# Optimization experiments

Measured on AMD Instinct MI355X. Metric: run time of the kernel, lower is better.

The kernel has to match this reference:

```python
import jax, jax.numpy as jnp
import numpy as np

N_NODES = 100000
N_EDGES = 1200000
F_IN, F_HID, F_OUT = 64, 16, 40


def setup_inputs() -> dict:
    key = jax.random.key(0)
    ks = jax.random.split(key, 6)
    x = jax.random.normal(ks[0], (N_NODES, F_IN), dtype=jnp.float32)
    edge_index = jax.random.randint(ks[1], (2, N_EDGES), 0, N_NODES, dtype=jnp.int32)
    s1 = 1.0 / np.sqrt(F_IN)
    s2 = 1.0 / np.sqrt(F_HID)
    return {
        "x": x,
        "edge_index": edge_index,
        "W1_self": jax.random.normal(ks[2], (F_IN, F_HID), dtype=jnp.float32) * s1,
        "W1_neigh": jax.random.normal(ks[3], (F_IN, F_HID), dtype=jnp.float32) * s1,
        "b1": jnp.zeros((F_HID,), dtype=jnp.float32),
        "W2_self": jax.random.normal(ks[4], (F_HID, F_OUT), dtype=jnp.float32) * s2,
        "W2_neigh": jax.random.normal(ks[5], (F_HID, F_OUT), dtype=jnp.float32) * s2,
        "b2": jnp.zeros((F_OUT,), dtype=jnp.float32),
    }


def _sage_conv(x, src, dst, W_self, W_neigh, b):
    # gather source features along edges, mean-aggregate onto destinations
    n = x.shape[0]
    deg = jax.ops.segment_sum(jnp.ones((src.shape[0],), x.dtype), dst, num_segments=n)
    agg = jax.ops.segment_sum(x[src], dst, num_segments=n)
    agg = agg / jnp.maximum(deg, 1.0)[:, None]
    return x @ W_self + agg @ W_neigh + b


def reference(x, edge_index, W1_self, W1_neigh, b1, W2_self, W2_neigh, b2):
    src, dst = edge_index[0], edge_index[1]
    h = jax.nn.relu(_sage_conv(x, src, dst, W1_self, W1_neigh, b1))
    # F.dropout with training=False is identity (eval-mode reference)
    out = _sage_conv(h, src, dst, W2_self, W2_neigh, b2)
    return jax.nn.log_softmax(out, axis=1)
```

## Files before the change

### kernel.cpp

```cpp
#include <hip/hip_runtime.h>
#include <math.h>

#define N_NODES 100000
#define N_EDGES 1200000
#define F_IN    64
#define F_HID   16
#define F_OUT   40

#define BK_SHIFT 7
#define BK_NODES 128
#define NB 782
#define CAP 1792
#define S1_EPB 8192
#define BIN_BLOCKS ((N_EDGES + S1_EPB - 1) / S1_EPB)
#define GEMM_BLOCKS ((N_NODES + 15) / 16)

typedef _Float16 v2h __attribute__((ext_vector_type(2)));

__global__ __launch_bounds__(256)
void k1_bin_gemm(const int* __restrict__ src, const int* __restrict__ dst,
                 unsigned* __restrict__ cursor, unsigned* __restrict__ csr,
                 const float* __restrict__ x, const float* __restrict__ Wn,
                 const float* __restrict__ Ws, const float* __restrict__ b1,
                 _Float16* __restrict__ t1, _Float16* __restrict__ xs, int nE) {
    __shared__ __align__(16) char smem[12416];
    int tid = threadIdx.x;
    int bid = blockIdx.x;
    if (bid < BIN_BLOCKS) {
        unsigned* cnt = (unsigned*)smem;
        for (int i = tid; i < NB; i += 256) cnt[i] = 0u;
        __syncthreads();
        int tb = bid * S1_EPB + tid * 32;
        if (tb + 32 <= nE) {
            const int4* d4 = (const int4*)(dst + tb);
#pragma unroll
            for (int j = 0; j < 8; j++) {
                int4 v = d4[j];
                atomicAdd(&cnt[((unsigned)v.x) >> BK_SHIFT], 1u);
                atomicAdd(&cnt[((unsigned)v.y) >> BK_SHIFT], 1u);
                atomicAdd(&cnt[((unsigned)v.z) >> BK_SHIFT], 1u);
                atomicAdd(&cnt[((unsigned)v.w) >> BK_SHIFT], 1u);
            }
        } else {
            for (int e = tb; e < nE && e < tb + 32; e++)
                atomicAdd(&cnt[((unsigned)dst[e]) >> BK_SHIFT], 1u);
        }
        __syncthreads();
        for (int i = tid; i < NB; i += 256) {
            unsigned c = cnt[i];
            cnt[i] = c ? atomicAdd(&cursor[i], c) : 0u;
        }
        __syncthreads();
        if (tb + 32 <= nE) {
            const int4* d4 = (const int4*)(dst + tb);
            const int4* s4 = (const int4*)(src + tb);
#pragma unroll
            for (int j = 0; j < 8; j++) {
                int4 dv = d4[j];
                int4 sv = s4[j];
                int da[4] = {dv.x, dv.y, dv.z, dv.w};
                int sa[4] = {sv.x, sv.y, sv.z, sv.w};
#pragma unroll
                for (int q = 0; q < 4; q++) {
                    unsigned d = (unsigned)da[q];
                    unsigned b = d >> BK_SHIFT;
                    unsigned pos = atomicAdd(&cnt[b], 1u);
                    if (pos < CAP)
                        csr[b * CAP + pos] = (((unsigned)sa[q]) << BK_SHIFT) | (d & (BK_NODES - 1));
                }
            }
        } else {
            for (int e = tb; e < nE && e < tb + 32; e++) {
                unsigned d = (unsigned)dst[e];
                unsigned b = d >> BK_SHIFT;
                unsigned pos = atomicAdd(&cnt[b], 1u);
                if (pos < CAP)
                    csr[b * CAP + pos] = (((unsigned)src[e]) << BK_SHIFT) | (d & (BK_NODES - 1));
            }
        }
    } else {
        float* sWn = (float*)smem;
        float* sWs = sWn + 1024;
        float* sb  = sWs + 1024;
        float* sx  = sb + 16;
        for (int i = tid; i < F_IN * F_HID; i += 256) { sWn[i] = Wn[i]; sWs[i] = Ws[i]; }
        if (tid < F_HID) sb[tid] = b1[tid];
        int row0 = (bid - BIN_BLOCKS) * 16;
        const float* xg = x + (size_t)row0 * F_IN;
        for (int i = tid; i < 16 * F_IN; i += 256)
            sx[(i >> 6) * 65 + (i & 63)] = xg[i];
        __syncthreads();
        int r = tid >> 4, c = tid & 15;
        int row = row0 + r;
        const float* xr = sx + r * 65;
        float sn = 0.f, ss = sb[c];
#pragma unroll
        for (int k = 0; k < F_IN; k++) {
            float xv = xr[k];
            sn += xv * sWn[k * F_HID + c];
            ss += xv * sWs[k * F_HID + c];
        }
        t1[row * F_HID + c] = (_Float16)sn;
        xs[row * F_HID + c] = (_Float16)ss;
    }
}

__global__ __launch_bounds__(256)
void k2_csr_sort(const unsigned* __restrict__ cursor, unsigned* __restrict__ csr,
                 unsigned* __restrict__ node_info) {
    __shared__ unsigned words[CAP];
    __shared__ unsigned hist[BK_NODES];
    __shared__ unsigned lcur[BK_NODES];
    int tid = threadIdx.x;
    int b = blockIdx.x;
    unsigned count = cursor[b]; if (count > CAP) count = CAP;
    unsigned* reg = csr + (size_t)b * CAP;
    for (unsigned i = tid; i < count; i += 256) words[i] = reg[i];
    for (int i = tid; i < BK_NODES; i += 256) hist[i] = 0u;
    __syncthreads();
    for (unsigned i = tid; i < count; i += 256)
        atomicAdd(&hist[words[i] & (BK_NODES - 1)], 1u);
    __syncthreads();
    unsigned hv = (tid < BK_NODES) ? hist[tid] : 0u;
    __syncthreads();
    for (int d = 1; d < BK_NODES; d <<= 1) {
        unsigned t = (tid < BK_NODES && tid >= d) ? hist[tid - d] : 0u;
        __syncthreads();
        if (tid < BK_NODES) hist[tid] += t;
        __syncthreads();
    }
    if (tid < BK_NODES) {
        unsigned excl = hist[tid] - hv;
        int node = (b << BK_SHIFT) + tid;
        if (node < N_NODES) node_info[node] = (excl << 16) | hv;
        lcur[tid] = excl;
    }
    __syncthreads();
    for (unsigned i = tid; i < count; i += 256) {
        unsigned w = words[i];
        unsigned pos = atomicAdd(&lcur[w & (BK_NODES - 1)], 1u);
        reg[pos] = w >> BK_SHIFT;
    }
}

__global__ __launch_bounds__(256)
void agg1_kernel(const unsigned* __restrict__ node_info, const unsigned* __restrict__ csr,
                 const _Float16* __restrict__ t1, _Float16* __restrict__ xsh, int n) {
    int g = blockIdx.x * 256 + threadIdx.x;
    int node = g >> 3;
    int f = g & 7;
    if (node >= n) return;
    unsigned info = node_info[node];
    int beg = (node >> BK_SHIFT) * CAP + (int)(info >> 16);
    int cnt = (int)(info & 0xFFFFu);
    int end = beg + cnt;
    const v2h* t2 = (const v2h*)t1;
    float ax = 0.f, ay = 0.f;
    int e = beg;
    for (; e + 4 <= end; e += 4) {
        unsigned s0 = csr[e], s1 = csr[e + 1], s2 = csr[e + 2], s3 = csr[e + 3];
        v2h v0 = t2[s0 * 8 + f], v1 = t2[s1 * 8 + f];
        v2h v2 = t2[s2 * 8 + f], v3 = t2[s3 * 8 + f];
        ax += (float)v0.x + (float)v1.x + (float)v2.x + (float)v3.x;
        ay += (float)v0.y + (float)v1.y + (float)v2.y + (float)v3.y;
    }
    for (; e < end; e++) {
        v2h v = t2[csr[e] * 8 + f];
        ax += (float)v.x; ay += (float)v.y;
    }
    float inv = 1.0f / fmaxf((float)cnt, 1.0f);
    v2h xv = ((const v2h*)xsh)[g];
    v2h hv;
    hv.x = (_Float16)fmaxf((float)xv.x + ax * inv, 0.f);
    hv.y = (_Float16)fmaxf((float)xv.y + ay * inv, 0.f);
    ((v2h*)xsh)[g] = hv;
}

__global__ __launch_bounds__(256)
void agg2_kernel(const unsigned* __restrict__ node_info, const unsigned* __restrict__ csr,
                 const _Float16* __restrict__ h,
                 const float* __restrict__ Ws, const float* __restrict__ Wn,
                 const float* __restrict__ b2, float* __restrict__ out, int n) {
    __shared__ float sWs[F_HID * F_OUT];
    __shared__ float sWn[F_HID * F_OUT];
    __shared__ float sb[F_OUT];
    int tid = threadIdx.x;
    for (int i = tid; i < F_HID * F_OUT; i += 256) { sWs[i] = Ws[i]; sWn[i] = Wn[i]; }
    if (tid < F_OUT) sb[tid] = b2[tid];
    __syncthreads();
    int g = blockIdx.x * 256 + tid;
    int node = g >> 3;
    int f = g & 7;
    if (node >= n) return;
    unsigned info = node_info[node];
    int beg = (node >> BK_SHIFT) * CAP + (int)(info >> 16);
    int cnt = (int)(info & 0xFFFFu);
    int end = beg + cnt;
    const v2h* h2 = (const v2h*)h;
    float ax = 0.f, ay = 0.f;
    int e = beg;
    for (; e + 4 <= end; e += 4) {
        unsigned s0 = csr[e], s1 = csr[e + 1], s2 = csr[e + 2], s3 = csr[e + 3];
        v2h v0 = h2[s0 * 8 + f], v1 = h2[s1 * 8 + f];
        v2h v2 = h2[s2 * 8 + f], v3 = h2[s3 * 8 + f];
        ax += (float)v0.x + (float)v1.x + (float)v2.x + (float)v3.x;
        ay += (float)v0.y + (float)v1.y + (float)v2.y + (float)v3.y;
    }
    for (; e < end; e++) {
        v2h v = h2[csr[e] * 8 + f];
        ax += (float)v.x; ay += (float)v.y;
    }
    float inv = 1.0f / fmaxf((float)cnt, 1.0f);
    ax *= inv; ay *= inv;
    v2h hs = h2[g];
    float hx = (float)hs.x, hy = (float)hs.y;
    float arow[F_HID], hrow[F_HID];
#pragma unroll
    for (int k = 0; k < 8; k++) {
        arow[2 * k]     = __shfl(ax, k, 8);
        arow[2 * k + 1] = __shfl(ay, k, 8);
        hrow[2 * k]     = __shfl(hx, k, 8);
        hrow[2 * k + 1] = __shfl(hy, k, 8);
    }
    float logit[5];
    float m = -INFINITY;
#pragma unroll
    for (int j = 0; j < 5; j++) {
        int c = j * 8 + f;
        float s = sb[c];
#pragma unroll
        for (int k = 0; k < F_HID; k++)
            s += hrow[k] * sWs[k * F_OUT + c] + arow[k] * sWn[k * F_OUT + c];
        logit[j] = s;
        m = fmaxf(m, s);
    }
    m = fmaxf(m, __shfl_xor(m, 1, 8));
    m = fmaxf(m, __shfl_xor(m, 2, 8));
    m = fmaxf(m, __shfl_xor(m, 4, 8));
    float sum = 0.f;
#pragma unroll
    for (int j = 0; j < 5; j++) sum += __expf(logit[j] - m);
    sum += __shfl_xor(sum, 1, 8);
    sum += __shfl_xor(sum, 2, 8);
    sum += __shfl_xor(sum, 4, 8);
    float lse = m + __logf(sum);
#pragma unroll
    for (int j = 0; j < 5; j++)
        out[node * F_OUT + j * 8 + f] = logit[j] - lse;
}

extern "C" void kernel_launch(void* const* d_in, const int* in_sizes, int n_in,
                              void* d_out, int out_size, void* d_ws, size_t ws_size,
                              hipStream_t stream) {
    const float* x        = (const float*)d_in[0];
    const int*   edges    = (const int*)d_in[1];
    const float* W1_self  = (const float*)d_in[2];
    const float* W1_neigh = (const float*)d_in[3];
    const float* b1       = (const float*)d_in[4];
    const float* W2_self  = (const float*)d_in[5];
    const float* W2_neigh = (const float*)d_in[6];
    const float* b2       = (const float*)d_in[7];
    float* out = (float*)d_out;

    const int* src = edges;
    const int* dst = edges + N_EDGES;

    char* base = (char*)d_ws;
    unsigned* cursor    = (unsigned*)base;
    unsigned* node_info = (unsigned*)(base + 4096);
    unsigned* csr       = (unsigned*)(base + 404608);
    _Float16* t1        = (_Float16*)(base + 6009984);
    _Float16* xsh       = (_Float16*)(base + 9209984);

    hipMemsetAsync(cursor, 0, 4096, stream);

    k1_bin_gemm<<<BIN_BLOCKS + GEMM_BLOCKS, 256, 0, stream>>>(
        src, dst, cursor, csr, x, W1_neigh, W1_self, b1, t1, xsh, N_EDGES);
    k2_csr_sort<<<NB, 256, 0, stream>>>(cursor, csr, node_info);
    agg1_kernel<<<(N_NODES * 8) / 256, 256, 0, stream>>>(node_info, csr, t1, xsh, N_NODES);
    agg2_kernel<<<(N_NODES * 8) / 256, 256, 0, stream>>>(node_info, csr, xsh,
                                                         W2_self, W2_neigh, b2, out, N_NODES);
}
```

Measured before the change: 165.8 us.

## Fuse bucket CSR sort with layer-1 aggregation and halve binning chunk size

Merges the per-bucket counting sort and the first-layer mean aggregation into one 512-thread kernel. The sorted neighbor list stays in shared memory and is read from there for aggregation, and is also written back to global memory for layer 2. This removes one launch and the global re-read of the CSR. Separately, the binning kernel now handles 4096 edges per block instead of 8192, which doubles the block count and adds more global cursor atomics. Aggregation now runs with only 782 blocks, and each thread handles two nodes, so there may be less latency hiding for the gathers.

After: 159.6 us. 3.8% less time.

```diff
diff --git a/kernel.cpp b/kernel.cpp
--- a/kernel.cpp
+++ b/kernel.cpp
@@ -11,7 +11,7 @@
 #define BK_NODES 128
 #define NB 782
 #define CAP 1792
-#define S1_EPB 8192
+#define S1_EPB 4096
 #define BIN_BLOCKS ((N_EDGES + S1_EPB - 1) / S1_EPB)
 #define GEMM_BLOCKS ((N_NODES + 15) / 16)
 
@@ -30,11 +30,11 @@
         unsigned* cnt = (unsigned*)smem;
         for (int i = tid; i < NB; i += 256) cnt[i] = 0u;
         __syncthreads();
-        int tb = bid * S1_EPB + tid * 32;
-        if (tb + 32 <= nE) {
+        int tb = bid * S1_EPB + tid * 16;
+        if (tb + 16 <= nE) {
             const int4* d4 = (const int4*)(dst + tb);
 #pragma unroll
-            for (int j = 0; j < 8; j++) {
+            for (int j = 0; j < 4; j++) {
                 int4 v = d4[j];
                 atomicAdd(&cnt[((unsigned)v.x) >> BK_SHIFT], 1u);
                 atomicAdd(&cnt[((unsigned)v.y) >> BK_SHIFT], 1u);
@@ -42,7 +42,7 @@
                 atomicAdd(&cnt[((unsigned)v.w) >> BK_SHIFT], 1u);
             }
         } else {
-            for (int e = tb; e < nE && e < tb + 32; e++)
+            for (int e = tb; e < nE && e < tb + 16; e++)
                 atomicAdd(&cnt[((unsigned)dst[e]) >> BK_SHIFT], 1u);
         }
         __syncthreads();
@@ -51,11 +51,11 @@
             cnt[i] = c ? atomicAdd(&cursor[i], c) : 0u;
         }
         __syncthreads();
-        if (tb + 32 <= nE) {
+        if (tb + 16 <= nE) {
             const int4* d4 = (const int4*)(dst + tb);
             const int4* s4 = (const int4*)(src + tb);
 #pragma unroll
-            for (int j = 0; j < 8; j++) {
+            for (int j = 0; j < 4; j++) {
                 int4 dv = d4[j];
                 int4 sv = s4[j];
                 int da[4] = {dv.x, dv.y, dv.z, dv.w};
@@ -70,7 +70,7 @@
                 }
             }
         } else {
-            for (int e = tb; e < nE && e < tb + 32; e++) {
+            for (int e = tb; e < nE && e < tb + 16; e++) {
                 unsigned d = (unsigned)dst[e];
                 unsigned b = d >> BK_SHIFT;
                 unsigned pos = atomicAdd(&cnt[b], 1u);
@@ -105,20 +105,23 @@
     }
 }
 
-__global__ __launch_bounds__(256)
-void k2_csr_sort(const unsigned* __restrict__ cursor, unsigned* __restrict__ csr,
-                 unsigned* __restrict__ node_info) {
+__global__ __launch_bounds__(512)
+void k2_sort_agg1(const unsigned* __restrict__ cursor, unsigned* __restrict__ csr,
+                  unsigned* __restrict__ node_info,
+                  const _Float16* __restrict__ t1, _Float16* __restrict__ xsh) {
     __shared__ unsigned words[CAP];
+    __shared__ unsigned sorted[CAP];
     __shared__ unsigned hist[BK_NODES];
     __shared__ unsigned lcur[BK_NODES];
+    __shared__ unsigned begs[BK_NODES];
     int tid = threadIdx.x;
     int b = blockIdx.x;
     unsigned count = cursor[b]; if (count > CAP) count = CAP;
     unsigned* reg = csr + (size_t)b * CAP;
-    for (unsigned i = tid; i < count; i += 256) words[i] = reg[i];
-    for (int i = tid; i < BK_NODES; i += 256) hist[i] = 0u;
-    __syncthreads();
-    for (unsigned i = tid; i < count; i += 256)
+    for (unsigned i = tid; i < count; i += 512) words[i] = reg[i];
+    if (tid < BK_NODES) hist[tid] = 0u;
+    __syncthreads();
+    for (unsigned i = tid; i < count; i += 512)
         atomicAdd(&hist[words[i] & (BK_NODES - 1)], 1u);
     __syncthreads();
     unsigned hv = (tid < BK_NODES) ? hist[tid] : 0u;
@@ -131,49 +134,52 @@
     }
     if (tid < BK_NODES) {
         unsigned excl = hist[tid] - hv;
+        begs[tid] = excl;
+        lcur[tid] = excl;
         int node = (b << BK_SHIFT) + tid;
         if (node < N_NODES) node_info[node] = (excl << 16) | hv;
-        lcur[tid] = excl;
-    }
-    __syncthreads();
-    for (unsigned i = tid; i < count; i += 256) {
+    }
+    __syncthreads();
+    for (unsigned i = tid; i < count; i += 512) {
         unsigned w = words[i];
         unsigned pos = atomicAdd(&lcur[w & (BK_NODES - 1)], 1u);
-        reg[pos] = w >> BK_SHIFT;
-    }
-}
-
-__global__ __launch_bounds__(256)
-void agg1_kernel(const unsigned* __restrict__ node_info, const unsigned* __restrict__ csr,
-                 const _Float16* __restrict__ t1, _Float16* __restrict__ xsh, int n) {
-    int g = blockIdx.x * 256 + threadIdx.x;
-    int node = g >> 3;
-    int f = g & 7;
-    if (node >= n) return;
-    unsigned info = node_info[node];
-    int beg = (node >> BK_SHIFT) * CAP + (int)(info >> 16);
-    int cnt = (int)(info & 0xFFFFu);
-    int end = beg + cnt;
+        sorted[pos] = w >> BK_SHIFT;
+    }
+    __syncthreads();
+    for (unsigned i = tid; i < count; i += 512) reg[i] = sorted[i];
+
+    int grp = tid >> 3;
+    int f = tid & 7;
     const v2h* t2 = (const v2h*)t1;
-    float ax = 0.f, ay = 0.f;
-    int e = beg;
-    for (; e + 4 <= end; e += 4) {
-        unsigned s0 = csr[e], s1 = csr[e + 1], s2 = csr[e + 2], s3 = csr[e + 3];
-        v2h v0 = t2[s0 * 8 + f], v1 = t2[s1 * 8 + f];
-        v2h v2 = t2[s2 * 8 + f], v3 = t2[s3 * 8 + f];
-        ax += (float)v0.x + (float)v1.x + (float)v2.x + (float)v3.x;
-        ay += (float)v0.y + (float)v1.y + (float)v2.y + (float)v3.y;
-    }
-    for (; e < end; e++) {
-        v2h v = t2[csr[e] * 8 + f];
-        ax += (float)v.x; ay += (float)v.y;
-    }
-    float inv = 1.0f / fmaxf((float)cnt, 1.0f);
-    v2h xv = ((const v2h*)xsh)[g];
-    v2h hv;
-    hv.x = (_Float16)fmaxf((float)xv.x + ax * inv, 0.f);
-    hv.y = (_Float16)fmaxf((float)xv.y + ay * inv, 0.f);
-    ((v2h*)xsh)[g] = hv;
+#pragma unroll
+    for (int half = 0; half < 2; half++) {
+        int ln = grp + half * 64;
+        int node = (b << BK_SHIFT) + ln;
+        if (node >= N_NODES) continue;
+        unsigned beg = begs[ln];
+        unsigned end = lcur[ln];
+        float ax = 0.f, ay = 0.f;
+        unsigned e = beg;
+        for (; e + 4 <= end; e += 4) {
+            unsigned s0 = sorted[e], s1 = sorted[e + 1];
+            unsigned s2 = sorted[e + 2], s3 = sorted[e + 3];
+            v2h v0 = t2[s0 * 8 + f], v1 = t2[s1 * 8 + f];
+            v2h v2 = t2[s2 * 8 + f], v3 = t2[s3 * 8 + f];
+            ax += (float)v0.x + (float)v1.x + (float)v2.x + (float)v3.x;
+            ay += (float)v0.y + (float)v1.y + (float)v2.y + (float)v3.y;
+        }
+        for (; e < end; e++) {
+            v2h v = t2[sorted[e] * 8 + f];
+            ax += (float)v.x; ay += (float)v.y;
+        }
+        float inv = 1.0f / fmaxf((float)(end - beg), 1.0f);
+        int g = node * 8 + f;
+        v2h xv = ((const v2h*)xsh)[g];
+        v2h hvv;
+        hvv.x = (_Float16)fmaxf((float)xv.x + ax * inv, 0.f);
+        hvv.y = (_Float16)fmaxf((float)xv.y + ay * inv, 0.f);
+        ((v2h*)xsh)[g] = hvv;
+    }
 }
 
 __global__ __launch_bounds__(256)
@@ -276,8 +282,7 @@
 
     k1_bin_gemm<<<BIN_BLOCKS + GEMM_BLOCKS, 256, 0, stream>>>(
         src, dst, cursor, csr, x, W1_neigh, W1_self, b1, t1, xsh, N_EDGES);
-    k2_csr_sort<<<NB, 256, 0, stream>>>(cursor, csr, node_info);
-    agg1_kernel<<<(N_NODES * 8) / 256, 256, 0, stream>>>(node_info, csr, t1, xsh, N_NODES);
+    k2_sort_agg1<<<NB, 512, 0, stream>>>(cursor, csr, node_info, t1, xsh);
     agg2_kernel<<<(N_NODES * 8) / 256, 256, 0, stream>>>(node_info, csr, xsh,
                                                          W2_self, W2_neigh, b2, out, N_NODES);
 }
```
